# Kernel optimization log

Measured on AMD Instinct MI355X. Metric: run time of the kernel, lower is better.

The kernel has to match this reference:

```python
import jax, jax.numpy as jnp
import numpy as np

EPS = 1e-5
S = 4        # s_scale
K = 3        # adjacency subsets
CB = 32      # per-branch channels


def _bn(x, g, b, m, v):
    # inference-mode BatchNorm2d over channel axis 1 of [n,c,t,v]
    scale = g * jax.lax.rsqrt(v + EPS)
    shift = b - m * scale
    return x * scale[None, :, None, None] + shift[None, :, None, None]


def _conv1x1(x, w, b):
    # pointwise conv: x [n,c,t,v], w [o,c], b [o]
    return jnp.einsum('nctv,oc->notv', x, w) + b[None, :, None, None]


def setup_inputs() -> dict:
    key = jax.random.key(0)
    ks = jax.random.split(key, 24)
    d = {}
    d['x'] = jax.random.normal(ks[0], (64, 256, 64, 25), jnp.float32)
    d['A'] = jax.random.uniform(ks[1], (K, 25, 25), jnp.float32)
    d['reduct_w'] = jax.random.normal(ks[2], (128, 256), jnp.float32) * 0.05
    d['reduct_b'] = jax.random.normal(ks[3], (128,), jnp.float32) * 0.05
    d['rg'] = jax.random.uniform(ks[4], (128,), jnp.float32) + 0.5
    d['rb'] = jax.random.normal(ks[5], (128,), jnp.float32) * 0.05
    d['rm'] = jax.random.normal(ks[6], (128,), jnp.float32) * 0.05
    d['rv'] = jax.random.uniform(ks[7], (128,), jnp.float32) + 0.5
    d['gcn_w'] = jax.random.normal(ks[8], (S, K * CB, CB), jnp.float32) * 0.1
    d['gcn_b'] = jax.random.normal(ks[9], (S, K * CB), jnp.float32) * 0.05
    d['PA'] = jax.random.normal(ks[10], (S, K, 25, 25), jnp.float32) * 0.05
    d['bg'] = jax.random.uniform(ks[11], (S, CB), jnp.float32) + 0.5
    d['bb'] = jax.random.normal(ks[12], (S, CB), jnp.float32) * 0.05
    d['bm'] = jax.random.normal(ks[13], (S, CB), jnp.float32) * 0.05
    d['bv'] = jax.random.uniform(ks[14], (S, CB), jnp.float32) + 0.5
    d['exp_w'] = jax.random.normal(ks[15], (256, 128), jnp.float32) * 0.05
    d['exp_b'] = jax.random.normal(ks[16], (256,), jnp.float32) * 0.05
    d['eg'] = jax.random.uniform(ks[17], (256,), jnp.float32) + 0.5
    d['eb'] = jax.random.normal(ks[18], (256,), jnp.float32) * 0.05
    d['em'] = jax.random.normal(ks[19], (256,), jnp.float32) * 0.05
    d['ev'] = jax.random.uniform(ks[20], (256,), jnp.float32) + 0.5
    return d


def reference(x, A, reduct_w, reduct_b, rg, rb, rm, rv, gcn_w, gcn_b, PA,
              bg, bb, bm, bv, exp_w, exp_b, eg, eb, em, ev):
    res = x  # identity residual (in_channels == out_channels)
    h = jax.nn.relu(_bn(_conv1x1(x, reduct_w, reduct_b), rg, rb, rm, rv))
    n, c, t, v = h.shape
    spx = jnp.split(h, S, axis=1)  # S chunks of CB channels
    outs = []
    sp = None
    for i in range(S):  # res2net sequential accumulation ('basic' mode)
        sp = spx[i] if i == 0 else sp + spx[i]
        g = _conv1x1(sp, gcn_w[i], gcn_b[i])           # [n, K*CB, t, v]
        g = g.reshape(n, K, CB, t, v)
        g = jnp.einsum('nkctv,kvw->nctw', g, A + PA[i])
        sp = jax.nn.relu(_bn(g, bg[i], bb[i], bm[i], bv[i]))
        outs.append(sp)
    h = jnp.concatenate(outs, axis=1)                  # [n, 4*CB, t, v]
    out = jax.nn.relu(_bn(_conv1x1(h, exp_w, exp_b), eg, eb, em, ev) + res)
    return out
```

## Files before the change

### kernel.cpp

```cpp
#include <hip/hip_runtime.h>
#include <cstdint>
#include <cstddef>

#define EPSV 1e-5f

using f32x4  = __attribute__((ext_vector_type(4))) float;
using bf16x8 = __attribute__((ext_vector_type(8))) short;

static __device__ __forceinline__ unsigned pk2(float lo, float hi) {
    unsigned a = __builtin_bit_cast(unsigned, lo);
    unsigned b = __builtin_bit_cast(unsigned, hi);
    a = (a + 0x7FFFu + ((a >> 16) & 1u)) >> 16;
    b = (b + 0x7FFFu + ((b >> 16) & 1u)) & 0xFFFF0000u;
    return a | b;
}
static __device__ __forceinline__ unsigned short bf16of(float v) {
    return (unsigned short)(pk2(v, 0.f) & 0xFFFFu);
}
static __device__ __forceinline__ void unpk2(unsigned u, float& lo, float& hi) {
    lo = __builtin_bit_cast(float, u << 16);
    hi = __builtin_bit_cast(float, u & 0xFFFF0000u);
}

__global__ __launch_bounds__(256) void prep_params(
    const float* __restrict__ rwb, const float* __restrict__ rg,
    const float* __restrict__ rb,  const float* __restrict__ rm,
    const float* __restrict__ rv,
    const float* __restrict__ ewb, const float* __restrict__ eg,
    const float* __restrict__ eb,  const float* __restrict__ em,
    const float* __restrict__ ev,
    const float* __restrict__ bg,  const float* __restrict__ bb,
    const float* __restrict__ bm,  const float* __restrict__ bv,
    float* __restrict__ prm)
{
    int t = threadIdx.x;
    if (t < 128) {
        float sc = rg[t] * rsqrtf(rv[t] + EPSV);
        prm[t]       = sc;
        prm[128 + t] = rb[t] - rm[t] * sc + rwb[t] * sc;
        float bsc = bg[t] * rsqrtf(bv[t] + EPSV);
        prm[768 + t] = bsc;
        prm[896 + t] = bb[t] - bm[t] * bsc;
    }
    {
        float sc = eg[t] * rsqrtf(ev[t] + EPSV);
        prm[256 + t] = sc;
        prm[512 + t] = eb[t] - em[t] * sc + ewb[t] * sc;
    }
}

template<int BMODE, int OUTMODE>
__global__ __launch_bounds__(256) void gemm_v2(
    const void* __restrict__ Bsrc,
    const float* __restrict__ Wt,
    const float* __restrict__ scale,
    const float* __restrict__ shift,
    const float* __restrict__ resid,
    void* __restrict__ OutP,
    int Cin, int O, int P)
{
    const int n    = blockIdx.z;
    const int p0   = blockIdx.x * 64;
    const int o0   = blockIdx.y * 128;
    const int tid  = threadIdx.x;
    const int lane = tid & 63;
    const int wid  = tid >> 6;
    const int wm   = wid >> 1, wn = wid & 1;
    const int rl   = lane & 15;

    __shared__ __align__(16) char smem[32768];
    short* sA = (short*)smem;

    f32x4 acc[4][2];
    #pragma unroll
    for (int i = 0; i < 4; ++i)
        #pragma unroll
        for (int j = 0; j < 2; ++j) acc[i][j] = (f32x4)0.f;

    for (int kc = 0; kc < Cin; kc += 64) {
        if (kc) __syncthreads();

        #pragma unroll
        for (int it = 0; it < 4; ++it) {
            int idx = tid + it * 256;
            int row = idx >> 3, k8 = (idx & 7) << 3;
            const float* wp = Wt + (size_t)(o0 + row) * Cin + kc + k8;
            float4 u = *(const float4*)wp;
            float4 v = *(const float4*)(wp + 4);
            uint4 w = make_uint4(pk2(u.x, u.y), pk2(u.z, u.w),
                                 pk2(v.x, v.y), pk2(v.z, v.w));
            *(uint4*)(&sA[(row << 6) + (k8 ^ ((row & 7) << 3))]) = w;
        }
        if constexpr (BMODE == 0) {
            float* sBf = (float*)(smem + 16384);
            #pragma unroll
            for (int it = 0; it < 4; ++it) {
                int idx = tid + it * 256;
                int k = idx >> 4, p4 = (idx & 15) << 2;
                float4 u = *(const float4*)((const float*)Bsrc
                    + (size_t)n * Cin * P + (size_t)(kc + k) * P + p0 + p4);
                *(float4*)(&sBf[(k << 6) + ((p4 + (((k >> 3) & 7) << 3)) & 63)]) = u;
            }
        } else {
            short* sB = (short*)(smem + 16384);
            #pragma unroll
            for (int it = 0; it < 2; ++it) {
                int idx = tid + it * 256;
                int p = idx >> 3, k8 = (idx & 7) << 3;
                uint4 w = *(const uint4*)((const unsigned short*)Bsrc
                    + ((size_t)n * P + p0 + p) * Cin + kc + k8);
                *(uint4*)(&sB[(p << 6) + (k8 ^ ((p & 7) << 3))]) = w;
            }
        }
        __syncthreads();

        #pragma unroll
        for (int ks = 0; ks < 2; ++ks) {
            const int k0 = ks * 32 + (lane >> 4) * 8;
            bf16x8 af[4], bfr[2];
            #pragma unroll
            for (int i = 0; i < 4; ++i) {
                int row = wm * 64 + i * 16 + rl;
                af[i] = *(const bf16x8*)(&sA[(row << 6) + (k0 ^ ((rl & 7) << 3))]);
            }
            if constexpr (BMODE == 0) {
                const float* sBf = (const float*)(smem + 16384);
                #pragma unroll
                for (int j = 0; j < 2; ++j) {
                    int p = wn * 32 + j * 16 + rl;
                    int base = (p + ((k0 >> 3) << 3)) & 63;
                    float f[8];
                    #pragma unroll
                    for (int q = 0; q < 8; ++q)
                        f[q] = sBf[((k0 + q) << 6) + base];
                    uint4 u = make_uint4(pk2(f[0], f[1]), pk2(f[2], f[3]),
                                         pk2(f[4], f[5]), pk2(f[6], f[7]));
                    bfr[j] = __builtin_bit_cast(bf16x8, u);
                }
            } else {
                const short* sB = (const short*)(smem + 16384);
                #pragma unroll
                for (int j = 0; j < 2; ++j) {
                    int p = wn * 32 + j * 16 + rl;
                    bfr[j] = *(const bf16x8*)(&sB[(p << 6) + (k0 ^ ((rl & 7) << 3))]);
                }
            }
            #pragma unroll
            for (int i = 0; i < 4; ++i)
                #pragma unroll
                for (int j = 0; j < 2; ++j)
                    acc[i][j] = __builtin_amdgcn_mfma_f32_16x16x32_bf16(
                        af[i], bfr[j], acc[i][j], 0, 0, 0);
        }
    }

    if constexpr (OUTMODE == 1) {
        __syncthreads();
        unsigned short* eL = (unsigned short*)smem;
        #pragma unroll
        for (int i = 0; i < 4; ++i) {
            #pragma unroll
            for (int r = 0; r < 4; ++r) {
                int ol = wm * 64 + i * 16 + (lane >> 4) * 4 + r;
                int o  = o0 + ol;
                float sc = scale[o], sh = shift[o];
                #pragma unroll
                for (int j = 0; j < 2; ++j) {
                    int p = wn * 32 + j * 16 + rl;
                    float v = fmaxf(fmaf(acc[i][j][r], sc, sh), 0.f);
                    eL[p * 128 + (ol ^ ((p & 15) << 3))] = bf16of(v);
                }
            }
        }
        __syncthreads();
        unsigned short* out = (unsigned short*)OutP;
        #pragma unroll
        for (int it = 0; it < 4; ++it) {
            int idx = tid + it * 256;
            int p = idx >> 4, m = idx & 15;
            uint4 u = *(const uint4*)(&eL[p * 128 + ((m ^ (p & 15)) << 3)]);
            *(uint4*)(out + ((size_t)n * P + p0 + p) * O + (m << 3)) = u;
        }
    } else {
        __syncthreads();
        float* eT = (float*)smem;
        #pragma unroll
        for (int i = 0; i < 4; ++i) {
            #pragma unroll
            for (int r = 0; r < 4; ++r) {
                int ol = wm * 64 + i * 16 + (lane >> 4) * 4 + r;
                int o  = o0 + ol;
                float sc = scale[o], sh = shift[o];
                #pragma unroll
                for (int j = 0; j < 2; ++j) {
                    int p = wn * 32 + j * 16 + rl;
                    eT[(ol << 6) + ((p + ((ol & 7) << 3)) & 63)] =
                        fmaf(acc[i][j][r], sc, sh);
                }
            }
        }
        __syncthreads();
        float* out = (float*)OutP;
        #pragma unroll
        for (int it = 0; it < 8; ++it) {
            int idx = tid + it * 256;
            int ol = idx >> 4, p4 = (idx & 15) << 2;
            float4 v = *(const float4*)(&eT[(ol << 6) + ((p4 + ((ol & 7) << 3)) & 63)]);
            size_t base = ((size_t)n * O + o0 + ol) * P + p0 + p4;
            if (resid) {
                float4 r4 = *(const float4*)(resid + base);
                v.x += r4.x; v.y += r4.y; v.z += r4.z; v.w += r4.w;
            }
            v.x = fmaxf(v.x, 0.f); v.y = fmaxf(v.y, 0.f);
            v.z = fmaxf(v.z, 0.f); v.w = fmaxf(v.w, 0.f);
            *(float4*)(out + base) = v;
        }
    }
}

__global__ __launch_bounds__(256) void gcn_step(
    const unsigned short* __restrict__ hT,
    unsigned short* __restrict__ outsT,
    const float* __restrict__ gw,
    const float* __restrict__ gb,
    const float* __restrict__ Aadj,
    const float* __restrict__ PAi,
    const float* __restrict__ bscale,
    const float* __restrict__ bshift,
    int step)
{
    const int n  = blockIdx.y;
    const int tt = blockIdx.x;
    const int tid = threadIdx.x;
    const int c  = tid & 31;
    const int tl = tid >> 5;

    __shared__ float smem[7200 + 3168 + 2100];
    float* sp  = smem;
    float* wsg = smem + 7200;
    float (*Mm)[25][28] = (float(*)[25][28])(smem + 7200 + 3168);
    unsigned short* outb = (unsigned short*)(smem + 7200);

    const size_t rowbase = (size_t)n * 1600 + (size_t)tt * 200;
    const unsigned short* hrow = hT + rowbase * 128 + step * 32;
    const unsigned short* prow = outsT + rowbase * 128 + (step - 1) * 32;

    for (int idx = tid; idx < 800; idx += 256) {
        int p = idx >> 2, c8 = (idx & 3) << 3;
        uint4 u = *(const uint4*)(hrow + (size_t)p * 128 + c8);
        float f[8];
        unpk2(u.x, f[0], f[1]); unpk2(u.y, f[2], f[3]);
        unpk2(u.z, f[4], f[5]); unpk2(u.w, f[6], f[7]);
        if (step > 0) {
            uint4 v = *(const uint4*)(prow + (size_t)p * 128 + c8);
            float g0, g1;
            unpk2(v.x, g0, g1); f[0] += g0; f[1] += g1;
            unpk2(v.y, g0, g1); f[2] += g0; f[3] += g1;
            unpk2(v.z, g0, g1); f[4] += g0; f[5] += g1;
            unpk2(v.w, g0, g1); f[6] += g0; f[7] += g1;
        }
        float* d = sp + p * 36 + c8;
        *(float4*)d       = make_float4(f[0], f[1], f[2], f[3]);
        *(float4*)(d + 4) = make_float4(f[4], f[5], f[6], f[7]);
    }
    for (int idx = tid; idx < 96 * 32; idx += 256)
        wsg[(idx >> 5) * 33 + (idx & 31)] = gw[idx];
    for (int idx = tid; idx < 3 * 625; idx += 256) {
        int k = idx / 625, rem = idx % 625;
        Mm[k][rem / 25][rem % 25] = Aadj[idx] + PAi[idx];
    }
    __syncthreads();

    float g[3][25];
    {
        float b0 = gb[c], b1 = gb[32 + c], b2 = gb[64 + c];
        #pragma unroll
        for (int v = 0; v < 25; ++v) { g[0][v] = b0; g[1][v] = b1; g[2][v] = b2; }
    }
    const float* srow = sp + tl * 25 * 36;
    for (int cin = 0; cin < 32; ++cin) {
        float w0 = wsg[c * 33 + cin];
        float w1 = wsg[(32 + c) * 33 + cin];
        float w2 = wsg[(64 + c) * 33 + cin];
        #pragma unroll
        for (int v = 0; v < 25; ++v) {
            float sv = srow[v * 36 + cin];
            g[0][v] = fmaf(w0, sv, g[0][v]);
            g[1][v] = fmaf(w1, sv, g[1][v]);
            g[2][v] = fmaf(w2, sv, g[2][v]);
        }
    }

    float out[25];
    #pragma unroll
    for (int w = 0; w < 25; ++w) out[w] = 0.f;
    #pragma unroll
    for (int k = 0; k < 3; ++k)
        #pragma unroll
        for (int v = 0; v < 25; ++v) {
            float gv = g[k][v];
            #pragma unroll
            for (int w = 0; w < 25; ++w)
                out[w] = fmaf(gv, Mm[k][v][w], out[w]);
        }

    float sc = bscale[c], sh = bshift[c];
    __syncthreads();
    #pragma unroll
    for (int w = 0; w < 25; ++w)
        outb[(tl * 25 + w) * 32 + c] = bf16of(fmaxf(fmaf(out[w], sc, sh), 0.f));
    __syncthreads();

    unsigned short* orow = outsT + rowbase * 128 + step * 32;
    for (int idx = tid; idx < 800; idx += 256) {
        int p = idx >> 2, c8 = (idx & 3) << 3;
        uint4 u = *(const uint4*)(&outb[p * 32 + c8]);
        *(uint4*)(orow + (size_t)p * 128 + c8) = u;
    }
}

extern "C" void kernel_launch(void* const* d_in, const int* in_sizes, int n_in,
                              void* d_out, int out_size, void* d_ws, size_t ws_size,
                              hipStream_t stream)
{
    const float* x   = (const float*)d_in[0];
    const float* A   = (const float*)d_in[1];
    const float* rw  = (const float*)d_in[2];
    const float* rwb = (const float*)d_in[3];
    const float* rg  = (const float*)d_in[4];
    const float* rb  = (const float*)d_in[5];
    const float* rm  = (const float*)d_in[6];
    const float* rv  = (const float*)d_in[7];
    const float* gw  = (const float*)d_in[8];
    const float* gb  = (const float*)d_in[9];
    const float* PA  = (const float*)d_in[10];
    const float* bg  = (const float*)d_in[11];
    const float* bb  = (const float*)d_in[12];
    const float* bm  = (const float*)d_in[13];
    const float* bv  = (const float*)d_in[14];
    const float* ew  = (const float*)d_in[15];
    const float* ewb = (const float*)d_in[16];
    const float* eg  = (const float*)d_in[17];
    const float* eb  = (const float*)d_in[18];
    const float* em  = (const float*)d_in[19];
    const float* ev  = (const float*)d_in[20];

    char* wsb = (char*)d_ws;
    unsigned short* hT    = (unsigned short*)wsb;
    unsigned short* outsT = (unsigned short*)(wsb + 26214400);
    float*          prm   = (float*)(wsb + 52428800);

    prep_params<<<1, 256, 0, stream>>>(rwb, rg, rb, rm, rv,
                                       ewb, eg, eb, em, ev,
                                       bg, bb, bm, bv, prm);

    gemm_v2<0, 1><<<dim3(25, 1, 64), 256, 0, stream>>>(
        x, rw, prm, prm + 128, nullptr, hT, 256, 128, 1600);

    for (int i = 0; i < 4; ++i) {
        gcn_step<<<dim3(8, 64), 256, 0, stream>>>(
            hT, outsT, gw + (size_t)i * 96 * 32, gb + (size_t)i * 96,
            A, PA + (size_t)i * 3 * 625,
            prm + 768 + i * 32, prm + 896 + i * 32, i);
    }

    gemm_v2<1, 0><<<dim3(25, 2, 64), 256, 0, stream>>>(
        outsT, ew, prm + 256, prm + 512, x, d_out, 128, 256, 1600);
}
```

Baseline: 209.6 us.

## Fuse four sequential GCN step launches into one kernel keeping state in LDS

Replaces four gcn_step launches with a single gcn_fused kernel that loops over the four res2net steps inside each block. The running sum sp stays in fp32 shared memory, so the previous step's bf16 output no longer has to be read back from global memory. This removes three launches and the re-reads of outsT, and it drops the bf16 rounding of the carried value. In exchange, each step adds an extra shared-memory write of out plus a barrier, and the grid is only 512 blocks, so the kernel runs serially longer per block.

```diff
diff --git a/kernel.cpp b/kernel.cpp
--- a/kernel.cpp
+++ b/kernel.cpp
@@ -218,16 +218,15 @@
     }
 }
 
-__global__ __launch_bounds__(256) void gcn_step(
+__global__ __launch_bounds__(256) void gcn_fused(
     const unsigned short* __restrict__ hT,
     unsigned short* __restrict__ outsT,
     const float* __restrict__ gw,
     const float* __restrict__ gb,
     const float* __restrict__ Aadj,
-    const float* __restrict__ PAi,
-    const float* __restrict__ bscale,
-    const float* __restrict__ bshift,
-    int step)
+    const float* __restrict__ PA,
+    const float* __restrict__ bsc4,
+    const float* __restrict__ bsh4)
 {
     const int n  = blockIdx.y;
     const int tt = blockIdx.x;
@@ -235,87 +234,114 @@
     const int c  = tid & 31;
     const int tl = tid >> 5;
 
-    __shared__ float smem[7200 + 3168 + 2100];
-    float* sp  = smem;
-    float* wsg = smem + 7200;
-    float (*Mm)[25][28] = (float(*)[25][28])(smem + 7200 + 3168);
-    unsigned short* outb = (unsigned short*)(smem + 7200);
+    __shared__ float sp[200 * 36];
+    __shared__ float wsg[96 * 33];
+    __shared__ float Mm[3][25][28];
+    __shared__ unsigned short outb[200 * 32];
 
     const size_t rowbase = (size_t)n * 1600 + (size_t)tt * 200;
-    const unsigned short* hrow = hT + rowbase * 128 + step * 32;
-    const unsigned short* prow = outsT + rowbase * 128 + (step - 1) * 32;
-
-    for (int idx = tid; idx < 800; idx += 256) {
-        int p = idx >> 2, c8 = (idx & 3) << 3;
-        uint4 u = *(const uint4*)(hrow + (size_t)p * 128 + c8);
-        float f[8];
-        unpk2(u.x, f[0], f[1]); unpk2(u.y, f[2], f[3]);
-        unpk2(u.z, f[4], f[5]); unpk2(u.w, f[6], f[7]);
-        if (step > 0) {
-            uint4 v = *(const uint4*)(prow + (size_t)p * 128 + c8);
-            float g0, g1;
-            unpk2(v.x, g0, g1); f[0] += g0; f[1] += g1;
-            unpk2(v.y, g0, g1); f[2] += g0; f[3] += g1;
-            unpk2(v.z, g0, g1); f[4] += g0; f[5] += g1;
-            unpk2(v.w, g0, g1); f[6] += g0; f[7] += g1;
-        }
-        float* d = sp + p * 36 + c8;
-        *(float4*)d       = make_float4(f[0], f[1], f[2], f[3]);
-        *(float4*)(d + 4) = make_float4(f[4], f[5], f[6], f[7]);
-    }
-    for (int idx = tid; idx < 96 * 32; idx += 256)
-        wsg[(idx >> 5) * 33 + (idx & 31)] = gw[idx];
-    for (int idx = tid; idx < 3 * 625; idx += 256) {
-        int k = idx / 625, rem = idx % 625;
-        Mm[k][rem / 25][rem % 25] = Aadj[idx] + PAi[idx];
+
+    {
+        const unsigned short* hrow = hT + rowbase * 128;
+        for (int idx = tid; idx < 800; idx += 256) {
+            int p = idx >> 2, c8 = (idx & 3) << 3;
+            uint4 u = *(const uint4*)(hrow + (size_t)p * 128 + c8);
+            float f[8];
+            unpk2(u.x, f[0], f[1]); unpk2(u.y, f[2], f[3]);
+            unpk2(u.z, f[4], f[5]); unpk2(u.w, f[6], f[7]);
+            float* d = sp + p * 36 + c8;
+            *(float4*)d       = make_float4(f[0], f[1], f[2], f[3]);
+            *(float4*)(d + 4) = make_float4(f[4], f[5], f[6], f[7]);
+        }
+        for (int idx = tid; idx < 96 * 32; idx += 256)
+            wsg[(idx >> 5) * 33 + (idx & 31)] = gw[idx];
+        for (int idx = tid; idx < 3 * 625; idx += 256) {
+            int k = idx / 625, rem = idx % 625;
+            Mm[k][rem / 25][rem % 25] = Aadj[idx] + PA[idx];
+        }
     }
     __syncthreads();
 
-    float g[3][25];
-    {
-        float b0 = gb[c], b1 = gb[32 + c], b2 = gb[64 + c];
-        #pragma unroll
-        for (int v = 0; v < 25; ++v) { g[0][v] = b0; g[1][v] = b1; g[2][v] = b2; }
-    }
-    const float* srow = sp + tl * 25 * 36;
-    for (int cin = 0; cin < 32; ++cin) {
-        float w0 = wsg[c * 33 + cin];
-        float w1 = wsg[(32 + c) * 33 + cin];
-        float w2 = wsg[(64 + c) * 33 + cin];
-        #pragma unroll
-        for (int v = 0; v < 25; ++v) {
-            float sv = srow[v * 36 + cin];
-            g[0][v] = fmaf(w0, sv, g[0][v]);
-            g[1][v] = fmaf(w1, sv, g[1][v]);
-            g[2][v] = fmaf(w2, sv, g[2][v]);
-        }
-    }
-
-    float out[25];
-    #pragma unroll
-    for (int w = 0; w < 25; ++w) out[w] = 0.f;
-    #pragma unroll
-    for (int k = 0; k < 3; ++k)
-        #pragma unroll
-        for (int v = 0; v < 25; ++v) {
-            float gv = g[k][v];
-            #pragma unroll
-            for (int w = 0; w < 25; ++w)
-                out[w] = fmaf(gv, Mm[k][v][w], out[w]);
-        }
-
-    float sc = bscale[c], sh = bshift[c];
-    __syncthreads();
-    #pragma unroll
-    for (int w = 0; w < 25; ++w)
-        outb[(tl * 25 + w) * 32 + c] = bf16of(fmaxf(fmaf(out[w], sc, sh), 0.f));
-    __syncthreads();
-
-    unsigned short* orow = outsT + rowbase * 128 + step * 32;
-    for (int idx = tid; idx < 800; idx += 256) {
-        int p = idx >> 2, c8 = (idx & 3) << 3;
-        uint4 u = *(const uint4*)(&outb[p * 32 + c8]);
-        *(uint4*)(orow + (size_t)p * 128 + c8) = u;
+    for (int step = 0; step < 4; ++step) {
+        float g[3][25];
+        {
+            const float* gbp = gb + step * 96;
+            float b0 = gbp[c], b1 = gbp[32 + c], b2 = gbp[64 + c];
+            #pragma unroll
+            for (int v = 0; v < 25; ++v) { g[0][v] = b0; g[1][v] = b1; g[2][v] = b2; }
+        }
+        const float* srow = sp + tl * 25 * 36;
+        for (int cin = 0; cin < 32; ++cin) {
+            float w0 = wsg[c * 33 + cin];
+            float w1 = wsg[(32 + c) * 33 + cin];
+            float w2 = wsg[(64 + c) * 33 + cin];
+            #pragma unroll
+            for (int v = 0; v < 25; ++v) {
+                float sv = srow[v * 36 + cin];
+                g[0][v] = fmaf(w0, sv, g[0][v]);
+                g[1][v] = fmaf(w1, sv, g[1][v]);
+                g[2][v] = fmaf(w2, sv, g[2][v]);
+            }
+        }
+
+        float out[25];
+        #pragma unroll
+        for (int w = 0; w < 25; ++w) out[w] = 0.f;
+        #pragma unroll
+        for (int k = 0; k < 3; ++k)
+            #pragma unroll
+            for (int v = 0; v < 25; ++v) {
+                float gv = g[k][v];
+                #pragma unroll
+                for (int w = 0; w < 25; ++w)
+                    out[w] = fmaf(gv, Mm[k][v][w], out[w]);
+            }
+
+        float sc = bsc4[step * 32 + c], sh = bsh4[step * 32 + c];
+        #pragma unroll
+        for (int w = 0; w < 25; ++w)
+            out[w] = fmaxf(fmaf(out[w], sc, sh), 0.f);
+
+        __syncthreads();
+
+        #pragma unroll
+        for (int w = 0; w < 25; ++w) {
+            sp[(tl * 25 + w) * 36 + c] = out[w];
+            outb[(tl * 25 + w) * 32 + c] = bf16of(out[w]);
+        }
+        __syncthreads();
+
+        {
+            unsigned short* orow = outsT + rowbase * 128 + step * 32;
+            for (int idx = tid; idx < 800; idx += 256) {
+                int p = idx >> 2, c8 = (idx & 3) << 3;
+                uint4 u = *(const uint4*)(&outb[p * 32 + c8]);
+                *(uint4*)(orow + (size_t)p * 128 + c8) = u;
+            }
+        }
+
+        if (step < 3) {
+            const unsigned short* hrow = hT + rowbase * 128 + (step + 1) * 32;
+            for (int idx = tid; idx < 800; idx += 256) {
+                int p = idx >> 2, c8 = (idx & 3) << 3;
+                uint4 u = *(const uint4*)(hrow + (size_t)p * 128 + c8);
+                float f[8];
+                unpk2(u.x, f[0], f[1]); unpk2(u.y, f[2], f[3]);
+                unpk2(u.z, f[4], f[5]); unpk2(u.w, f[6], f[7]);
+                float* d = sp + p * 36 + c8;
+                #pragma unroll
+                for (int q = 0; q < 8; ++q) d[q] += f[q];
+            }
+            const float* gwp = gw + (step + 1) * 96 * 32;
+            for (int idx = tid; idx < 96 * 32; idx += 256)
+                wsg[(idx >> 5) * 33 + (idx & 31)] = gwp[idx];
+            const float* pap = PA + (step + 1) * 3 * 625;
+            for (int idx = tid; idx < 3 * 625; idx += 256) {
+                int k = idx / 625, rem = idx % 625;
+                Mm[k][rem / 25][rem % 25] = Aadj[idx] + pap[idx];
+            }
+            __syncthreads();
+        }
     }
 }
 
@@ -357,12 +383,8 @@
     gemm_v2<0, 1><<<dim3(25, 1, 64), 256, 0, stream>>>(
         x, rw, prm, prm + 128, nullptr, hT, 256, 128, 1600);
 
-    for (int i = 0; i < 4; ++i) {
-        gcn_step<<<dim3(8, 64), 256, 0, stream>>>(
-            hT, outsT, gw + (size_t)i * 96 * 32, gb + (size_t)i * 96,
-            A, PA + (size_t)i * 3 * 625,
-            prm + 768 + i * 32, prm + 896 + i * 32, i);
-    }
+    gcn_fused<<<dim3(8, 64), 256, 0, stream>>>(
+        hT, outsT, gw, gb, A, PA, prm + 768, prm + 896);
 
     gemm_v2<1, 0><<<dim3(25, 2, 64), 256, 0, stream>>>(
         outsT, ew, prm + 256, prm + 512, x, d_out, 128, 256, 1600);
```

After: 187.7 us. 10.5% less time.
